# Kernel optimization log

Hardware: AMD Instinct MI355X
Metric: run time of the kernel (lower is better)

## Reference

```python
import jax, jax.numpy as jnp
import numpy as np

N_NODES = 100000


def _gcn_conv(x, edge_index, W, b, n_nodes):
    # PyG GCNConv with add_self_loops=True, default gcn_norm:
    #   out = D^{-1/2} (A + I) D^{-1/2} (x @ W) + b
    xw = x @ W  # [N, out_dim]
    src = jnp.concatenate([edge_index[0], jnp.arange(n_nodes)])
    dst = jnp.concatenate([edge_index[1], jnp.arange(n_nodes)])
    ones = jnp.ones(src.shape[0], dtype=x.dtype)
    deg = jax.ops.segment_sum(ones, dst, num_segments=n_nodes)  # includes self loops
    dinv = jnp.where(deg > 0, jax.lax.rsqrt(deg), 0.0)
    norm = dinv[src] * dinv[dst]  # [E + N]
    msgs = xw[src] * norm[:, None]  # gather + scale per edge
    out = jax.ops.segment_sum(msgs, dst, num_segments=n_nodes)
    return out + b


def setup_inputs() -> dict:
    key = jax.random.key(0)
    k1, k2, k3, k4 = jax.random.split(key, 4)
    N, E = N_NODES, 1600000
    in_dim, hid_dim, out_dim = 128, 128, 64
    x = jax.random.normal(k1, (N, in_dim), dtype=jnp.float32)
    edge_index = jax.random.randint(k2, (2, E), 0, N, dtype=jnp.int64)
    W1 = jax.random.normal(k3, (in_dim, hid_dim), dtype=jnp.float32) * (1.0 / np.sqrt(in_dim))
    b1 = jnp.zeros((hid_dim,), dtype=jnp.float32)
    W2 = jax.random.normal(k4, (hid_dim, out_dim), dtype=jnp.float32) * (1.0 / np.sqrt(hid_dim))
    b2 = jnp.zeros((out_dim,), dtype=jnp.float32)
    return {"x": x, "edge_index": edge_index, "W1": W1, "b1": b1, "W2": W2, "b2": b2}


def reference(x, edge_index, W1, b1, W2, b2):
    h = _gcn_conv(x, edge_index, W1, b1, N_NODES)
    out = _gcn_conv(h, edge_index, W2, b2, N_NODES)
    return out
```

## Files before the change

kernel.cpp:

```cpp
#include <hip/hip_runtime.h>

#define NNODES 100000
#define NBUCK ((NNODES + 127) >> 7)
#define CAPB 3072
#define BINCAP 16
#define GFILL 256

typedef __attribute__((ext_vector_type(8))) short short8;
typedef __attribute__((ext_vector_type(4))) float f32x4;

__device__ __forceinline__ float bf2f(unsigned short u) {
    unsigned int v = ((unsigned int)u) << 16;
    return __builtin_bit_cast(float, v);
}
__device__ __forceinline__ unsigned short f2bf(float f) {
    unsigned int u = __builtin_bit_cast(unsigned int, f);
    u += 0x7FFF + ((u >> 16) & 1);
    return (unsigned short)(u >> 16);
}


__global__ __launch_bounds__(512) void fill_wc(const int* __restrict__ ei, int E,
                                               int* __restrict__ gcur,
                                               int* __restrict__ seg) {
    __shared__ int lcnt[NBUCK];
    __shared__ int lbin[NBUCK * BINCAP];

    const int t = threadIdx.x;
    for (int i = t; i < NBUCK; i += 512) lcnt[i] = 0;
    __syncthreads();

    const int per = (E + GFILL - 1) / GFILL;
    const int e0 = blockIdx.x * per;
    const int e1 = min(e0 + per, E);

    for (int base = e0; base < e1; base += 1024) {
#pragma unroll
        for (int u = 0; u < 2; ++u) {
            int e = base + u * 512 + t;
            if (e < e1) {
                int src = ei[e];
                int d = ei[E + e];
                int b = (unsigned)d >> 7;
                int p = (src << 7) | (d & 127);
                int pos = atomicAdd(&lcnt[b], 1);
                if (pos < BINCAP) {
                    lbin[b * BINCAP + pos] = p;
                } else {
                    int gp = atomicAdd(&gcur[b << 4], 1);
                    if (gp < CAPB) seg[b * CAPB + gp] = p;
                }
            }
        }
        __syncthreads();
        for (int bb = t; bb < NBUCK; bb += 512) {
            if (lcnt[bb] >= BINCAP) {
                int gp = atomicAdd(&gcur[bb << 4], BINCAP);
                if (gp + BINCAP <= CAPB) {
                    int* dp = seg + bb * CAPB + gp;
                    const int* sp = lbin + bb * BINCAP;
#pragma unroll
                    for (int j = 0; j < BINCAP; ++j) dp[j] = sp[j];
                }
                lcnt[bb] = 0;
            }
        }
        __syncthreads();
    }
    for (int bb = t; bb < NBUCK; bb += 512) {
        int c = min(lcnt[bb], BINCAP);
        if (c > 0) {
            int gp = atomicAdd(&gcur[bb << 4], c);
            int* dp = seg + bb * CAPB;
            const int* sp = lbin + bb * BINCAP;
            for (int j = 0; j < c && gp + j < CAPB; ++j) dp[gp + j] = sp[j];
        }
    }
}


__global__ __launch_bounds__(512) void sortseg(const int* __restrict__ gcur,
                                               int* __restrict__ seg,
                                               float* __restrict__ dinv,
                                               int* __restrict__ rsb,
                                               int* __restrict__ cntb, int N) {
    __shared__ int el[CAPB];
    __shared__ int csr[CAPB];
    __shared__ int cnt[128], sh[128], rs[128], cur[128];

    const int t = threadIdx.x, b = blockIdx.x;
    const int total = min(gcur[b << 4], CAPB);

    if (t < 128) cnt[t] = 0;
    __syncthreads();
    {
        const int* sp = seg + b * CAPB;
        for (int i = t; i < total; i += 512) el[i] = sp[i];
    }
    __syncthreads();

    for (int i = t; i < total; i += 512) atomicAdd(&cnt[el[i] & 127], 1);
    __syncthreads();
    int v = (t < 128) ? cnt[t] : 0;
    if (t < 128) sh[t] = v;
    __syncthreads();
    for (int offp = 1; offp < 128; offp <<= 1) {
        int u = (t < 128 && t >= offp) ? sh[t - offp] : 0;
        __syncthreads();
        if (t < 128) sh[t] += u;
        __syncthreads();
    }
    if (t < 128) {
        int excl = sh[t] - v;
        rs[t] = excl;
        cur[t] = excl;
    }
    __syncthreads();
    for (int i = t; i < total; i += 512) {
        int p = el[i];
        int pos = atomicAdd(&cur[p & 127], 1);
        csr[pos] = (int)((unsigned)p >> 7);
    }
    __syncthreads();

    {
        int* dp = seg + b * CAPB;
        for (int i = t; i < total; i += 512) dp[i] = csr[i];
    }
    if (t < 128) {
        rsb[b * 128 + t] = rs[t];
        cntb[b * 128 + t] = cnt[t];
        int node = (b << 7) + t;
        if (node < N) dinv[node] = rsqrtf((float)cnt[t] + 1.0f);
    }
}


__global__ __launch_bounds__(256) void w12_kernel(const float* __restrict__ W1,
                                                  const float* __restrict__ b1,
                                                  const float* __restrict__ W2,
                                                  float* __restrict__ W12,
                                                  float* __restrict__ bW2,
                                                  unsigned short* __restrict__ whi,
                                                  unsigned short* __restrict__ wlo) {
    int j = threadIdx.x % 64;
    int r = threadIdx.x / 64;
    if (blockIdx.x < 32) {
        int i = blockIdx.x * 4 + r;
        float acc = 0.f;
        for (int k = 0; k < 128; ++k) acc += W1[i * 128 + k] * W2[k * 64 + j];
        W12[i * 64 + j] = acc;
        int kc = i >> 5;
        int ik = i & 31;
        int lane = ((ik >> 3) << 4) | (j & 15);
        int jj = ik & 7;
        int nt = j >> 4;
        size_t idx = (size_t)(((nt << 2) | kc) * 64 + lane) * 8 + jj;
        unsigned short h = f2bf(acc);
        whi[idx] = h;
        wlo[idx] = f2bf(acc - bf2f(h));
    } else if (r == 0) {
        float acc = 0.f;
        for (int k = 0; k < 128; ++k) acc += b1[k] * W2[k * 64 + j];
        bW2[j] = acc;
    }
}


__global__ __launch_bounds__(256) void gemm_mfma(const float* __restrict__ X,
                                                 const unsigned short* __restrict__ whi,
                                                 const unsigned short* __restrict__ wlo,
                                                 const float* __restrict__ dinv,
                                                 unsigned short* __restrict__ Ybf, int N) {
    const int tid = threadIdx.x;
    const int wv = tid >> 6;
    const int l = tid & 63;
    const int lm = l & 15;
    const int lk = l >> 4;
    const int rowbase = blockIdx.x * 64 + wv * 16;
    const int arow = min(rowbase + lm, N - 1);

    const float* xp = X + (size_t)arow * 128 + lk * 8;

    f32x4 acc[4];
#pragma unroll
    for (int nt = 0; nt < 4; ++nt) acc[nt] = (f32x4){0.f, 0.f, 0.f, 0.f};

#pragma unroll
    for (int kc = 0; kc < 4; ++kc) {
        float4 xa = *(const float4*)(xp + kc * 32);
        float4 xb = *(const float4*)(xp + kc * 32 + 4);
        float xs[8] = {xa.x, xa.y, xa.z, xa.w, xb.x, xb.y, xb.z, xb.w};
        short8 ah, al;
#pragma unroll
        for (int j = 0; j < 8; ++j) {
            unsigned short h = f2bf(xs[j]);
            ah[j] = (short)h;
            al[j] = (short)f2bf(xs[j] - bf2f(h));
        }
#pragma unroll
        for (int nt = 0; nt < 4; ++nt) {
            const size_t fb = (size_t)(((nt << 2) | kc) * 64 + l) * 8;
            short8 bh = *(const short8*)(whi + fb);
            short8 bl = *(const short8*)(wlo + fb);
            acc[nt] = __builtin_amdgcn_mfma_f32_16x16x32_bf16(ah, bh, acc[nt], 0, 0, 0);
            acc[nt] = __builtin_amdgcn_mfma_f32_16x16x32_bf16(ah, bl, acc[nt], 0, 0, 0);
            acc[nt] = __builtin_amdgcn_mfma_f32_16x16x32_bf16(al, bh, acc[nt], 0, 0, 0);
        }
    }

#pragma unroll
    for (int i = 0; i < 4; ++i) {
        int r = rowbase + lk * 4 + i;
        if (r < N) {
            float dv = dinv[r];
#pragma unroll
            for (int nt = 0; nt < 4; ++nt)
                Ybf[(size_t)r * 64 + nt * 16 + lm] = f2bf(acc[nt][i] * dv);
        }
    }
}


template <bool FINAL>
__global__ __launch_bounds__(256, 8) void agg_csr(const int* __restrict__ seg,
                                                  const int* __restrict__ rsb,
                                                  const int* __restrict__ cntb,
                                                  const unsigned short* __restrict__ Y,
                                                  const float* __restrict__ dinv,
                                                  const float* __restrict__ bW2,
                                                  const float* __restrict__ b2,
                                                  unsigned short* __restrict__ out_bf,
                                                  float* __restrict__ out_f, int N) {
    __shared__ int csrS[CAPB];
    __shared__ int rsS[32], cntS[32];

    const int t = threadIdx.x;
    const int b = blockIdx.x >> 2;
    const int q = blockIdx.x & 3;
    const int nb = q << 5;

    if (t < 32) {
        rsS[t] = rsb[b * 128 + nb + t];
        cntS[t] = cntb[b * 128 + nb + t];
    }
    __syncthreads();
    const int start = rsS[0];
    const int L = rsS[31] + cntS[31] - start;
    {
        const int* sp = seg + (size_t)b * CAPB + start;
        for (int i = t; i < L; i += 256) csrS[i] = sp[i];
    }
    __syncthreads();

    const int g = t >> 3, lane = t & 7, c8 = lane * 8;
    const int node = (b << 7) + nb + g;
    if (node >= N) return;

    float a[8];
    {
        short8 sv = *(const short8*)(Y + (size_t)node * 64 + c8);
#pragma unroll
        for (int j = 0; j < 8; ++j) a[j] = bf2f((unsigned short)sv[j]);
    }
    float ds = 0.f;

    const int s0 = rsS[g] - start;
    const int ne = cntS[g];
    const int e0 = s0 + ne;
    int i = s0;

    for (; i + 8 <= e0; i += 8) {
        int a0 = csrS[i + 0];
        int a1 = csrS[i + 1];
        int a2 = csrS[i + 2];
        int a3 = csrS[i + 3];
        int a4 = csrS[i + 4];
        int a5 = csrS[i + 5];
        int a6 = csrS[i + 6];
        int a7 = csrS[i + 7];
        short8 v0 = *(const short8*)(Y + (size_t)a0 * 64 + c8);
        short8 v1 = *(const short8*)(Y + (size_t)a1 * 64 + c8);
        short8 v2 = *(const short8*)(Y + (size_t)a2 * 64 + c8);
        short8 v3 = *(const short8*)(Y + (size_t)a3 * 64 + c8);
        short8 v4 = *(const short8*)(Y + (size_t)a4 * 64 + c8);
        short8 v5 = *(const short8*)(Y + (size_t)a5 * 64 + c8);
        short8 v6 = *(const short8*)(Y + (size_t)a6 * 64 + c8);
        short8 v7 = *(const short8*)(Y + (size_t)a7 * 64 + c8);
        if (FINAL) ds += dinv[csrS[i + lane]];
#pragma unroll
        for (int j = 0; j < 8; ++j) {
            a[j] += bf2f((unsigned short)v0[j]) + bf2f((unsigned short)v1[j])
                  + bf2f((unsigned short)v2[j]) + bf2f((unsigned short)v3[j])
                  + bf2f((unsigned short)v4[j]) + bf2f((unsigned short)v5[j])
                  + bf2f((unsigned short)v6[j]) + bf2f((unsigned short)v7[j]);
        }
    }
    for (; i + 4 <= e0; i += 4) {
        int a0 = csrS[i + 0];
        int a1 = csrS[i + 1];
        int a2 = csrS[i + 2];
        int a3 = csrS[i + 3];
        short8 v0 = *(const short8*)(Y + (size_t)a0 * 64 + c8);
        short8 v1 = *(const short8*)(Y + (size_t)a1 * 64 + c8);
        short8 v2 = *(const short8*)(Y + (size_t)a2 * 64 + c8);
        short8 v3 = *(const short8*)(Y + (size_t)a3 * 64 + c8);
        if (FINAL && lane < 4) ds += dinv[csrS[i + lane]];
#pragma unroll
        for (int j = 0; j < 8; ++j) {
            a[j] += bf2f((unsigned short)v0[j]) + bf2f((unsigned short)v1[j])
                  + bf2f((unsigned short)v2[j]) + bf2f((unsigned short)v3[j]);
        }
    }
    for (; i < e0; ++i) {
        int aa = csrS[i];
        short8 vv = *(const short8*)(Y + (size_t)aa * 64 + c8);
        if (FINAL && lane == 0) ds += dinv[aa];
#pragma unroll
        for (int j = 0; j < 8; ++j) a[j] += bf2f((unsigned short)vv[j]);
    }

    float di = rsqrtf((float)ne + 1.0f);
    if (FINAL) {
        float dt = ds;
        dt += __shfl_xor(dt, 1, 64);
        dt += __shfl_xor(dt, 2, 64);
        dt += __shfl_xor(dt, 4, 64);
        float si = di * (di + dt);
        float4 bb0 = *(const float4*)(bW2 + c8);
        float4 bb1 = *(const float4*)(bW2 + c8 + 4);
        float4 bv0 = *(const float4*)(b2 + c8);
        float4 bv1 = *(const float4*)(b2 + c8 + 4);
        float4 o0, o1;
        o0.x = di * a[0] + si * bb0.x + bv0.x;
        o0.y = di * a[1] + si * bb0.y + bv0.y;
        o0.z = di * a[2] + si * bb0.z + bv0.z;
        o0.w = di * a[3] + si * bb0.w + bv0.w;
        o1.x = di * a[4] + si * bb1.x + bv1.x;
        o1.y = di * a[5] + si * bb1.y + bv1.y;
        o1.z = di * a[6] + si * bb1.z + bv1.z;
        o1.w = di * a[7] + si * bb1.w + bv1.w;
        *(float4*)(out_f + (size_t)node * 64 + c8) = o0;
        *(float4*)(out_f + (size_t)node * 64 + c8 + 4) = o1;
    } else {
        float d2 = di * di;
        short8 o;
#pragma unroll
        for (int j = 0; j < 8; ++j) o[j] = (short)f2bf(d2 * a[j]);
        *(short8*)(out_bf + (size_t)node * 64 + c8) = o;
    }
}


extern "C" void kernel_launch(void* const* d_in, const int* in_sizes, int n_in,
                              void* d_out, int out_size, void* d_ws, size_t ws_size,
                              hipStream_t stream) {
    const float* x  = (const float*)d_in[0];
    const int*   ei = (const int*)d_in[1];
    const float* W1 = (const float*)d_in[2];
    const float* b1 = (const float*)d_in[3];
    const float* W2 = (const float*)d_in[4];
    const float* b2 = (const float*)d_in[5];
    float* out = (float*)d_out;

    const int N = NNODES;
    const int E = in_sizes[1] / 2;

    float* ws   = (float*)d_ws;
    float* dinv = ws;
    float* W12  = dinv + N;
    float* bW2  = W12 + 8192;
    unsigned short* whi = (unsigned short*)(bW2 + 64);
    unsigned short* wlo = whi + 8192;
    unsigned short* ybf = wlo + 8192;
    unsigned short* zbf = ybf + (size_t)N * 64;
    int*  seg  = (int*)(zbf + (size_t)N * 64);
    int*  gcur = seg + (size_t)NBUCK * CAPB;
    int*  rsb  = gcur + (size_t)NBUCK * 16;
    int*  cntb = rsb + (size_t)NBUCK * 128;

    hipMemsetAsync(gcur, 0, (size_t)NBUCK * 16 * sizeof(int), stream);

    fill_wc<<<GFILL, 512, 0, stream>>>(ei, E, gcur, seg);
    w12_kernel<<<33, 256, 0, stream>>>(W1, b1, W2, W12, bW2, whi, wlo);
    sortseg<<<NBUCK, 512, 0, stream>>>(gcur, seg, dinv, rsb, cntb, N);

    gemm_mfma<<<(N + 63) / 64, 256, 0, stream>>>(x, whi, wlo, dinv, ybf, N);
    agg_csr<false><<<NBUCK * 4, 256, 0, stream>>>(seg, rsb, cntb, ybf, dinv, nullptr, nullptr, zbf, nullptr, N);
    agg_csr<true><<<NBUCK * 4, 256, 0, stream>>>(seg, rsb, cntb, zbf, dinv, bW2, b2, nullptr, out, N);
}
```

Baseline: 212.0 us.

## Fuse bucket sort into first aggregation and precompute dinv neighbor sums

```diff
diff --git a/kernel.cpp b/kernel.cpp
--- a/kernel.cpp
+++ b/kernel.cpp
@@ -79,56 +79,19 @@
 }
 
 
-__global__ __launch_bounds__(512) void sortseg(const int* __restrict__ gcur,
-                                               int* __restrict__ seg,
-                                               float* __restrict__ dinv,
-                                               int* __restrict__ rsb,
-                                               int* __restrict__ cntb, int N) {
-    __shared__ int el[CAPB];
-    __shared__ int csr[CAPB];
-    __shared__ int cnt[128], sh[128], rs[128], cur[128];
-
+__global__ __launch_bounds__(256) void stats_kernel(const int* __restrict__ gcur,
+                                                    const int* __restrict__ seg,
+                                                    int* __restrict__ cntb,
+                                                    float* __restrict__ dinv, int N) {
+    __shared__ int cnt[128];
     const int t = threadIdx.x, b = blockIdx.x;
-    const int total = min(gcur[b << 4], CAPB);
-
     if (t < 128) cnt[t] = 0;
     __syncthreads();
-    {
-        const int* sp = seg + b * CAPB;
-        for (int i = t; i < total; i += 512) el[i] = sp[i];
-    }
-    __syncthreads();
-
-    for (int i = t; i < total; i += 512) atomicAdd(&cnt[el[i] & 127], 1);
-    __syncthreads();
-    int v = (t < 128) ? cnt[t] : 0;
-    if (t < 128) sh[t] = v;
-    __syncthreads();
-    for (int offp = 1; offp < 128; offp <<= 1) {
-        int u = (t < 128 && t >= offp) ? sh[t - offp] : 0;
-        __syncthreads();
-        if (t < 128) sh[t] += u;
-        __syncthreads();
-    }
+    int c = min(gcur[b << 4], CAPB);
+    const int* sp = seg + (size_t)b * CAPB;
+    for (int i = t; i < c; i += 256) atomicAdd(&cnt[sp[i] & 127], 1);
+    __syncthreads();
     if (t < 128) {
-        int excl = sh[t] - v;
-        rs[t] = excl;
-        cur[t] = excl;
-    }
-    __syncthreads();
-    for (int i = t; i < total; i += 512) {
-        int p = el[i];
-        int pos = atomicAdd(&cur[p & 127], 1);
-        csr[pos] = (int)((unsigned)p >> 7);
-    }
-    __syncthreads();
-
-    {
-        int* dp = seg + b * CAPB;
-        for (int i = t; i < total; i += 512) dp[i] = csr[i];
-    }
-    if (t < 128) {
-        rsb[b * 128 + t] = rs[t];
         cntb[b * 128 + t] = cnt[t];
         int node = (b << 7) + t;
         if (node < N) dinv[node] = rsqrtf((float)cnt[t] + 1.0f);
@@ -222,16 +185,153 @@
 }
 
 
-template <bool FINAL>
-__global__ __launch_bounds__(256, 8) void agg_csr(const int* __restrict__ seg,
-                                                  const int* __restrict__ rsb,
+__global__ __launch_bounds__(512) void agg1_fused(const int* __restrict__ gcur,
+                                                  int* __restrict__ seg,
                                                   const int* __restrict__ cntb,
+                                                  const float* __restrict__ dinv,
                                                   const unsigned short* __restrict__ Y,
-                                                  const float* __restrict__ dinv,
-                                                  const float* __restrict__ bW2,
-                                                  const float* __restrict__ b2,
-                                                  unsigned short* __restrict__ out_bf,
-                                                  float* __restrict__ out_f, int N) {
+                                                  int* __restrict__ rsb,
+                                                  float* __restrict__ dsum,
+                                                  unsigned short* __restrict__ out_bf, int N) {
+    __shared__ int el[CAPB];
+    __shared__ int csr[CAPB];
+    __shared__ int cnt[128], sh[128], rs[128], cur[128];
+
+    const int t = threadIdx.x, b = blockIdx.x;
+    const int total = min(gcur[b << 4], CAPB);
+
+    if (t < 128) cnt[t] = cntb[b * 128 + t];
+    {
+        const int* sp = seg + (size_t)b * CAPB;
+        for (int i = t; i < total; i += 512) el[i] = sp[i];
+    }
+    __syncthreads();
+
+    int v = (t < 128) ? cnt[t] : 0;
+    if (t < 128) sh[t] = v;
+    __syncthreads();
+    for (int offp = 1; offp < 128; offp <<= 1) {
+        int u = (t < 128 && t >= offp) ? sh[t - offp] : 0;
+        __syncthreads();
+        if (t < 128) sh[t] += u;
+        __syncthreads();
+    }
+    if (t < 128) {
+        int excl = sh[t] - v;
+        rs[t] = excl;
+        cur[t] = excl;
+    }
+    __syncthreads();
+
+    for (int i = t; i < total; i += 512) {
+        int p = el[i];
+        int pos = atomicAdd(&cur[p & 127], 1);
+        csr[pos] = (int)((unsigned)p >> 7);
+    }
+    __syncthreads();
+
+    {
+        int* dp = seg + (size_t)b * CAPB;
+        for (int i = t; i < total; i += 512) dp[i] = csr[i];
+    }
+    if (t < 128) rsb[b * 128 + t] = rs[t];
+
+    const int g = t >> 3, lane = t & 7, c8 = lane * 8;
+    const int base = b << 7;
+
+#pragma unroll
+    for (int k = 0; k < 2; ++k) {
+        const int nl = g + (k << 6);
+        const int node = base + nl;
+        if (node >= N) continue;
+
+        float a[8];
+        {
+            short8 sv = *(const short8*)(Y + (size_t)node * 64 + c8);
+#pragma unroll
+            for (int j = 0; j < 8; ++j) a[j] = bf2f((unsigned short)sv[j]);
+        }
+        float ds = 0.f;
+
+        const int s0 = rs[nl];
+        const int ne = cnt[nl];
+        const int e0 = s0 + ne;
+        int i = s0;
+
+        for (; i + 8 <= e0; i += 8) {
+            int a0 = csr[i + 0];
+            int a1 = csr[i + 1];
+            int a2 = csr[i + 2];
+            int a3 = csr[i + 3];
+            int a4 = csr[i + 4];
+            int a5 = csr[i + 5];
+            int a6 = csr[i + 6];
+            int a7 = csr[i + 7];
+            short8 v0 = *(const short8*)(Y + (size_t)a0 * 64 + c8);
+            short8 v1 = *(const short8*)(Y + (size_t)a1 * 64 + c8);
+            short8 v2 = *(const short8*)(Y + (size_t)a2 * 64 + c8);
+            short8 v3 = *(const short8*)(Y + (size_t)a3 * 64 + c8);
+            short8 v4 = *(const short8*)(Y + (size_t)a4 * 64 + c8);
+            short8 v5 = *(const short8*)(Y + (size_t)a5 * 64 + c8);
+            short8 v6 = *(const short8*)(Y + (size_t)a6 * 64 + c8);
+            short8 v7 = *(const short8*)(Y + (size_t)a7 * 64 + c8);
+            ds += dinv[csr[i + lane]];
+#pragma unroll
+            for (int j = 0; j < 8; ++j) {
+                a[j] += bf2f((unsigned short)v0[j]) + bf2f((unsigned short)v1[j])
+                      + bf2f((unsigned short)v2[j]) + bf2f((unsigned short)v3[j])
+                      + bf2f((unsigned short)v4[j]) + bf2f((unsigned short)v5[j])
+                      + bf2f((unsigned short)v6[j]) + bf2f((unsigned short)v7[j]);
+            }
+        }
+        for (; i + 4 <= e0; i += 4) {
+            int a0 = csr[i + 0];
+            int a1 = csr[i + 1];
+            int a2 = csr[i + 2];
+            int a3 = csr[i + 3];
+            short8 v0 = *(const short8*)(Y + (size_t)a0 * 64 + c8);
+            short8 v1 = *(const short8*)(Y + (size_t)a1 * 64 + c8);
+            short8 v2 = *(const short8*)(Y + (size_t)a2 * 64 + c8);
+            short8 v3 = *(const short8*)(Y + (size_t)a3 * 64 + c8);
+            if (lane < 4) ds += dinv[csr[i + lane]];
+#pragma unroll
+            for (int j = 0; j < 8; ++j) {
+                a[j] += bf2f((unsigned short)v0[j]) + bf2f((unsigned short)v1[j])
+                      + bf2f((unsigned short)v2[j]) + bf2f((unsigned short)v3[j]);
+            }
+        }
+        for (; i < e0; ++i) {
+            int aa = csr[i];
+            short8 vv = *(const short8*)(Y + (size_t)aa * 64 + c8);
+            if (lane == 0) ds += dinv[aa];
+#pragma unroll
+            for (int j = 0; j < 8; ++j) a[j] += bf2f((unsigned short)vv[j]);
+        }
+
+        float dt = ds;
+        dt += __shfl_xor(dt, 1, 64);
+        dt += __shfl_xor(dt, 2, 64);
+        dt += __shfl_xor(dt, 4, 64);
+        if (lane == 0) dsum[node] = dt;
+
+        float di = rsqrtf((float)ne + 1.0f);
+        float d2 = di * di;
+        short8 o;
+#pragma unroll
+        for (int j = 0; j < 8; ++j) o[j] = (short)f2bf(d2 * a[j]);
+        *(short8*)(out_bf + (size_t)node * 64 + c8) = o;
+    }
+}
+
+
+__global__ __launch_bounds__(256, 8) void agg2(const int* __restrict__ seg,
+                                               const int* __restrict__ rsb,
+                                               const int* __restrict__ cntb,
+                                               const unsigned short* __restrict__ Y,
+                                               const float* __restrict__ dsum,
+                                               const float* __restrict__ bW2,
+                                               const float* __restrict__ b2,
+                                               float* __restrict__ out_f, int N) {
     __shared__ int csrS[CAPB];
     __shared__ int rsS[32], cntS[32];
 
@@ -263,7 +363,6 @@
 #pragma unroll
         for (int j = 0; j < 8; ++j) a[j] = bf2f((unsigned short)sv[j]);
     }
-    float ds = 0.f;
 
     const int s0 = rsS[g] - start;
     const int ne = cntS[g];
@@ -287,7 +386,6 @@
         short8 v5 = *(const short8*)(Y + (size_t)a5 * 64 + c8);
         short8 v6 = *(const short8*)(Y + (size_t)a6 * 64 + c8);
         short8 v7 = *(const short8*)(Y + (size_t)a7 * 64 + c8);
-        if (FINAL) ds += dinv[csrS[i + lane]];
 #pragma unroll
         for (int j = 0; j < 8; ++j) {
             a[j] += bf2f((unsigned short)v0[j]) + bf2f((unsigned short)v1[j])
@@ -305,7 +403,6 @@
         short8 v1 = *(const short8*)(Y + (size_t)a1 * 64 + c8);
         short8 v2 = *(const short8*)(Y + (size_t)a2 * 64 + c8);
         short8 v3 = *(const short8*)(Y + (size_t)a3 * 64 + c8);
-        if (FINAL && lane < 4) ds += dinv[csrS[i + lane]];
 #pragma unroll
         for (int j = 0; j < 8; ++j) {
             a[j] += bf2f((unsigned short)v0[j]) + bf2f((unsigned short)v1[j])
@@ -315,40 +412,27 @@
     for (; i < e0; ++i) {
         int aa = csrS[i];
         short8 vv = *(const short8*)(Y + (size_t)aa * 64 + c8);
-        if (FINAL && lane == 0) ds += dinv[aa];
 #pragma unroll
         for (int j = 0; j < 8; ++j) a[j] += bf2f((unsigned short)vv[j]);
     }
 
     float di = rsqrtf((float)ne + 1.0f);
-    if (FINAL) {
-        float dt = ds;
-        dt += __shfl_xor(dt, 1, 64);
-        dt += __shfl_xor(dt, 2, 64);
-        dt += __shfl_xor(dt, 4, 64);
-        float si = di * (di + dt);
-        float4 bb0 = *(const float4*)(bW2 + c8);
-        float4 bb1 = *(const float4*)(bW2 + c8 + 4);
-        float4 bv0 = *(const float4*)(b2 + c8);
-        float4 bv1 = *(const float4*)(b2 + c8 + 4);
-        float4 o0, o1;
-        o0.x = di * a[0] + si * bb0.x + bv0.x;
-        o0.y = di * a[1] + si * bb0.y + bv0.y;
-        o0.z = di * a[2] + si * bb0.z + bv0.z;
-        o0.w = di * a[3] + si * bb0.w + bv0.w;
-        o1.x = di * a[4] + si * bb1.x + bv1.x;
-        o1.y = di * a[5] + si * bb1.y + bv1.y;
-        o1.z = di * a[6] + si * bb1.z + bv1.z;
-        o1.w = di * a[7] + si * bb1.w + bv1.w;
-        *(float4*)(out_f + (size_t)node * 64 + c8) = o0;
-        *(float4*)(out_f + (size_t)node * 64 + c8 + 4) = o1;
-    } else {
-        float d2 = di * di;
-        short8 o;
-#pragma unroll
-        for (int j = 0; j < 8; ++j) o[j] = (short)f2bf(d2 * a[j]);
-        *(short8*)(out_bf + (size_t)node * 64 + c8) = o;
-    }
+    float si = di * (di + dsum[node]);
+    float4 bb0 = *(const float4*)(bW2 + c8);
+    float4 bb1 = *(const float4*)(bW2 + c8 + 4);
+    float4 bv0 = *(const float4*)(b2 + c8);
+    float4 bv1 = *(const float4*)(b2 + c8 + 4);
+    float4 o0, o1;
+    o0.x = di * a[0] + si * bb0.x + bv0.x;
+    o0.y = di * a[1] + si * bb0.y + bv0.y;
+    o0.z = di * a[2] + si * bb0.z + bv0.z;
+    o0.w = di * a[3] + si * bb0.w + bv0.w;
+    o1.x = di * a[4] + si * bb1.x + bv1.x;
+    o1.y = di * a[5] + si * bb1.y + bv1.y;
+    o1.z = di * a[6] + si * bb1.z + bv1.z;
+    o1.w = di * a[7] + si * bb1.w + bv1.w;
+    *(float4*)(out_f + (size_t)node * 64 + c8) = o0;
+    *(float4*)(out_f + (size_t)node * 64 + c8 + 4) = o1;
 }
 
 
@@ -368,7 +452,8 @@
 
     float* ws   = (float*)d_ws;
     float* dinv = ws;
-    float* W12  = dinv + N;
+    float* dsum = dinv + N;
+    float* W12  = dsum + N;
     float* bW2  = W12 + 8192;
     unsigned short* whi = (unsigned short*)(bW2 + 64);
     unsigned short* wlo = whi + 8192;
@@ -383,9 +468,9 @@
 
     fill_wc<<<GFILL, 512, 0, stream>>>(ei, E, gcur, seg);
     w12_kernel<<<33, 256, 0, stream>>>(W1, b1, W2, W12, bW2, whi, wlo);
-    sortseg<<<NBUCK, 512, 0, stream>>>(gcur, seg, dinv, rsb, cntb, N);
+    stats_kernel<<<NBUCK, 256, 0, stream>>>(gcur, seg, cntb, dinv, N);
 
     gemm_mfma<<<(N + 63) / 64, 256, 0, stream>>>(x, whi, wlo, dinv, ybf, N);
-    agg_csr<false><<<NBUCK * 4, 256, 0, stream>>>(seg, rsb, cntb, ybf, dinv, nullptr, nullptr, zbf, nullptr, N);
-    agg_csr<true><<<NBUCK * 4, 256, 0, stream>>>(seg, rsb, cntb, zbf, dinv, bW2, b2, nullptr, out, N);
-}
+    agg1_fused<<<NBUCK, 512, 0, stream>>>(gcur, seg, cntb, dinv, ybf, rsb, dsum, zbf, N);
+    agg2<<<NBUCK * 4, 256, 0, stream>>>(seg, rsb, cntb, zbf, dsum, bW2, b2, out, N);
+}
```

Result: no change. 214.0 us (+0.9%).
